# Kernel optimization log

Measured on AMD Instinct MI355X. Metric: run time of the kernel, lower is better.

The kernel has to match this reference:

```python
import jax, jax.numpy as jnp
import numpy as np

B, S, D = 8, 1024, 1024

def setup_inputs() -> dict:
    key = jax.random.key(0)
    ks = jax.random.split(key, 6)
    context = jax.random.normal(ks[0], (B, S, D), dtype=jnp.float32)
    eos_mask = jax.random.randint(ks[1], (B, S), 0, 2, dtype=jnp.int32)
    prior = jax.random.uniform(ks[2], (), dtype=jnp.float32)
    adj_mat = jax.random.randint(ks[3], (B, S, S), 0, 2, dtype=jnp.int32)
    Wk = jax.random.normal(ks[4], (D, D), dtype=jnp.float32) * 0.02
    Wq = jax.random.normal(ks[5], (D, D), dtype=jnp.float32) * 0.02
    bk = jnp.zeros((D,), jnp.float32)
    bq = jnp.zeros((D,), jnp.float32)
    ln_gamma = jnp.ones((D,), jnp.float32)
    ln_beta = jnp.zeros((D,), jnp.float32)
    return {"context": context, "eos_mask": eos_mask, "prior": prior,
            "adj_mat": adj_mat, "Wk": Wk, "bk": bk, "Wq": Wq, "bq": bq,
            "ln_gamma": ln_gamma, "ln_beta": ln_beta}

def reference(context, eos_mask, prior, adj_mat, Wk, bk, Wq, bq, ln_gamma, ln_beta):
    d_model = context.shape[-1]
    seq_len = context.shape[1]
    # LayerNorm (annotated-transformer style: unbiased std, eps added to std)
    mu = jnp.mean(context, axis=-1, keepdims=True)
    std = jnp.std(context, axis=-1, keepdims=True, ddof=1)
    x = ln_gamma * (context - mu) / (std + 1e-6) + ln_beta
    # projections (torch Linear: x @ W.T + b)
    key_p = x @ Wk.T + bk
    query = x @ Wq.T + bq
    scores = jnp.einsum('bqd,bkd->bqk', query, key_p) / (d_model / 2)
    scores = jnp.where(adj_mat == 0, -1e9, scores)
    neibor_attn = jax.nn.softmax(scores, axis=-1)
    neibor_attn = jnp.sqrt(neibor_attn * jnp.swapaxes(neibor_attn, -1, -2) + 1e-9)
    neibor_attn = prior + (1.0 - prior) * neibor_attn
    # constant structural matrices
    a = jnp.eye(seq_len, k=1, dtype=jnp.float32)          # superdiagonal
    b = jnp.eye(seq_len, dtype=jnp.float32)               # diagonal
    tri = jnp.triu(jnp.ones((seq_len, seq_len), jnp.float32))  # upper incl diag
    # t = (log(attn+eps) masked to superdiagonal) @ tri
    t = jnp.matmul(jnp.where(a == 0, 0.0, jnp.log(neibor_attn + 1e-9)), tri)
    g_attn = jnp.exp(jnp.matmul(tri, t))
    g_attn = jnp.where((tri - b) == 0, 0.0, g_attn)  # keep strict upper only
    g_attn = g_attn + jnp.swapaxes(g_attn, -1, -2) + jnp.where(b == 0, 1e-9, neibor_attn)
    return (g_attn, neibor_attn)
```

## Files before the change

kernel.cpp:

```cpp
#include <hip/hip_runtime.h>
#include <hip/hip_bf16.h>

#define S_LEN 1024
#define D_DIM 1024
#define N_BAT 8
#define BSS   (8ull*1024ull*1024ull)

using bf16x8 = __attribute__((ext_vector_type(8))) short;
using f32x4  = __attribute__((ext_vector_type(4))) float;

__device__ __forceinline__ short f2bf(float v) {
    __hip_bfloat16 h = __float2bfloat16(v);
    return *reinterpret_cast<short*>(&h);
}

__device__ __forceinline__ void gload_lds16(const void* g, void* l) {
    __builtin_amdgcn_global_load_lds(
        (const __attribute__((address_space(1))) void*)g,
        (__attribute__((address_space(3))) void*)l, 16, 0, 0);
}

#define RDFRAG(slot, AF, BF)                                                  \
    {                                                                         \
        const char* _Ac = (const char*)As + (slot) * 32768;                   \
        const char* _Bc = (const char*)Bs + (slot) * 16384;                   \
        _Pragma("unroll")                                                     \
        for (int _m = 0; _m < 4; ++_m) {                                      \
            const int _row = wr * 64 + _m * 16 + rsel;                        \
            _Pragma("unroll")                                                 \
            for (int _kk = 0; _kk < 2; ++_kk)                                 \
                AF[_m][_kk] = *(const bf16x8*)&_Ac[_row * 128 +               \
                                                  ((_kk * 64 + kb) ^ sw)];    \
        }                                                                     \
        _Pragma("unroll")                                                     \
        for (int _n = 0; _n < 4; ++_n) {                                      \
            const int _row = wc * 64 + _n * 16 + rsel;                        \
            _Pragma("unroll")                                                 \
            for (int _kk = 0; _kk < 2; ++_kk)                                 \
                BF[_n][_kk] = *(const bf16x8*)&_Bc[_row * 128 +               \
                                                  ((_kk * 64 + kb) ^ sw)];    \
        }                                                                     \
    }

#define MMA_ALL(AF, BF)                                                       \
    __builtin_amdgcn_s_setprio(1);                                            \
    _Pragma("unroll")                                                         \
    for (int _kk = 0; _kk < 2; ++_kk)                                         \
        _Pragma("unroll")                                                     \
        for (int _m = 0; _m < 4; ++_m)                                        \
            _Pragma("unroll")                                                  \
            for (int _n = 0; _n < 4; ++_n)                                    \
                acc[_m][_n] = __builtin_amdgcn_mfma_f32_16x16x32_bf16(        \
                    AF[_m][_kk], BF[_n][_kk], acc[_m][_n], 0, 0, 0);          \
    __builtin_amdgcn_s_setprio(0);

template<int KITERS>
__device__ __forceinline__ void gemm_mainloop256(
    const short* __restrict__ A, const short* __restrict__ Bt,
    int brow, int bcol, int kstart,
    short* As, short* Bs, f32x4 acc[4][4])
{
    const int tid  = threadIdx.x;
    const int lane = tid & 63;
    const int w    = tid >> 6;
    const int wr   = w >> 1;
    const int wc   = w & 1;
    const int rsel = lane & 15;
    const int kb   = (lane >> 4) * 16;
    const int sw   = (rsel & 7) << 4;

    const int srow  = tid >> 3;
    const int scolb = ((tid & 7) * 16) ^ ((srow & 7) << 4);
    const int sdst  = tid * 16;

#pragma unroll
    for (int m = 0; m < 4; ++m)
#pragma unroll
        for (int n = 0; n < 4; ++n) acc[m][n] = 0.0f;

    auto stage = [&](int slot, int k0) {
        char* Ad = (char*)As + slot * 32768;
        char* Bd = (char*)Bs + slot * 16384;
#pragma unroll
        for (int c = 0; c < 4; ++c) {
            const int row = c * 64 + srow;
            gload_lds16((const char*)(A + (size_t)(brow + row) * 1024 + k0) + scolb,
                        Ad + c * 8192 + sdst);
        }
#pragma unroll
        for (int c = 0; c < 2; ++c) {
            const int row = c * 64 + srow;
            gload_lds16((const char*)(Bt + (size_t)(bcol + row) * 1024 + k0) + scolb,
                        Bd + c * 8192 + sdst);
        }
    };

    stage(0, kstart);
    if (KITERS > 1) {
        stage(1, kstart + 64);
        asm volatile("s_waitcnt vmcnt(6)" ::: "memory");
    } else {
        asm volatile("s_waitcnt vmcnt(0)" ::: "memory");
    }
    __builtin_amdgcn_s_barrier();
    asm volatile("" ::: "memory");

    bf16x8 af0[4][2], bf0[4][2], af1[4][2], bf1[4][2];
    RDFRAG(0, af0, bf0);

#pragma unroll
    for (int t = 0; t < KITERS; ++t) {
        if (t + 2 < KITERS) stage((t + 2) % 3, kstart + (t + 2) * 64);
        if (t + 2 < KITERS)      asm volatile("s_waitcnt vmcnt(6)" ::: "memory");
        else if (t + 1 < KITERS) asm volatile("s_waitcnt vmcnt(0)" ::: "memory");
        if (t + 1 < KITERS) {
            asm volatile("s_waitcnt lgkmcnt(0)" ::: "memory");
            __builtin_amdgcn_s_barrier();
            asm volatile("" ::: "memory");
            if ((t & 1) == 0) { RDFRAG((t + 1) % 3, af1, bf1); }
            else              { RDFRAG((t + 1) % 3, af0, bf0); }
        }
        if ((t & 1) == 0) { MMA_ALL(af0, bf0); }
        else              { MMA_ALL(af1, bf1); }
    }
}

__global__ __launch_bounds__(256) void pack_adj(
    const int* __restrict__ adj, unsigned* __restrict__ mb)
{
    const int lane = threadIdx.x & 63;
    const size_t wid = ((size_t)blockIdx.x * 256 + threadIdx.x) >> 6;
    const size_t nw  = ((size_t)gridDim.x * 256) >> 6;
    for (size_t c = wid; c < (BSS >> 6); c += nw) {
        const int a = adj[(c << 6) + lane];
        const unsigned long long m = __ballot(a != 0);
        if ((lane & 31) == 0)
            mb[(c << 1) + (lane >> 5)] = (unsigned)(m >> (lane & 32));
    }
}

__global__ __launch_bounds__(512) void gemm_bf16(
    const short* __restrict__ A, const short* __restrict__ Bt,
    short* __restrict__ C)
{
    __shared__ char smem[147456];
    short* As = (short*)smem;
    short* Bs = (short*)(smem + 98304);
    const int flat = blockIdx.x + 32 * blockIdx.y;
    const int nid  = (flat & 7) * 32 + (flat >> 3);
    const int mx   = nid >> 3;
    const int ny   = nid & 7;
    const int brow = mx * 256, bcol = ny * 128;

    f32x4 acc[4][4];
    gemm_mainloop256<16>(A, Bt, brow, bcol, 0, As, Bs, acc);

    __syncthreads();
    short* ep = (short*)smem;
    const int lane = threadIdx.x & 63;
    const int w    = threadIdx.x >> 6;
    const int wr   = w >> 1, wc = w & 1;
#pragma unroll
    for (int m = 0; m < 4; ++m)
#pragma unroll
        for (int n = 0; n < 4; ++n) {
            const int Cc = wc * 64 + n * 16 + (lane & 15);
#pragma unroll
            for (int r = 0; r < 4; ++r) {
                const int R = wr * 64 + m * 16 + (lane >> 4) * 4 + r;
                ep[R * 136 + Cc] = f2bf(acc[m][n][r]);
            }
        }
    __syncthreads();
#pragma unroll
    for (int it = 0; it < 8; ++it) {
        const int fl  = it * 512 + threadIdx.x;
        const int row = fl >> 4;
        const int c8  = fl & 15;
        const bf16x8 v = *(const bf16x8*)&ep[row * 136 + c8 * 8];
        *(bf16x8*)&C[(size_t)(brow + row) * 1024 + bcol + c8 * 8] = v;
    }
}

__global__ __launch_bounds__(512) void gemm_scores(
    const short* __restrict__ Tm, const short* __restrict__ Xm,
    const float* __restrict__ p, const float* __restrict__ r2,
    const float* __restrict__ c0p, const unsigned* __restrict__ mbase,
    float* __restrict__ Sc)
{
    __shared__ char smem[147456];
    short* As = (short*)smem;
    short* Bs = (short*)(smem + 98304);
    const int flat = blockIdx.x + 4 * blockIdx.y + 32 * blockIdx.z;
    const int nid  = (flat & 7) * 32 + (flat >> 3);
    const int b    = nid >> 5;
    const int rem  = nid & 31;
    const int mx   = rem & 3;
    const int ny   = rem >> 2;
    const short* A  = Tm + (size_t)b * 1024 * 1024;
    const short* Bt = Xm + (size_t)b * 1024 * 1024;
    const float* pb = p  + (size_t)b * 1024;
    const float* rb = r2 + (size_t)b * 1024;
    const unsigned* mbb = mbase + (size_t)b * 32768;
    float* C = Sc + (size_t)b * 1024 * 1024;
    const int brow = mx * 256, bcol = ny * 128;

    f32x4 acc[4][4];
    gemm_mainloop256<16>(A, Bt, brow, bcol, 0, As, Bs, acc);

    __syncthreads();
    float* ep = (float*)smem;
    const int lane = threadIdx.x & 63;
    const int w    = threadIdx.x >> 6;
    const int wr   = w >> 1, wc = w & 1;
#pragma unroll
    for (int m = 0; m < 4; ++m)
#pragma unroll
        for (int n = 0; n < 4; ++n) {
            const int Cc = wc * 64 + n * 16 + (lane & 15);
#pragma unroll
            for (int r = 0; r < 4; ++r) {
                const int R = wr * 64 + m * 16 + (lane >> 4) * 4 + r;
                ep[R * 132 + Cc] = acc[m][n][r];
            }
        }
    __syncthreads();
    const float c0v = c0p[0];
#pragma unroll
    for (int it = 0; it < 16; ++it) {
        const int fl   = it * 512 + threadIdx.x;
        const int row  = fl >> 5;
        const int col4 = fl & 31;
        const int rowg = brow + row;
        const int colg = bcol + col4 * 4;
        float4 v = *(const float4*)&ep[row * 132 + col4 * 4];
        const float4 rv = *(const float4*)&rb[colg];
        const float pa = pb[rowg] + c0v;
        const unsigned mw = mbb[rowg * 32 + (bcol >> 5) + (col4 >> 3)];
        const int j0 = (col4 & 7) * 4;
        v.x = ((mw >> (j0 + 0)) & 1) ? (v.x + pa + rv.x) * 0.001953125f : -1e9f;
        v.y = ((mw >> (j0 + 1)) & 1) ? (v.y + pa + rv.y) * 0.001953125f : -1e9f;
        v.z = ((mw >> (j0 + 2)) & 1) ? (v.z + pa + rv.z) * 0.001953125f : -1e9f;
        v.w = ((mw >> (j0 + 3)) & 1) ? (v.w + pa + rv.w) * 0.001953125f : -1e9f;
        *(float4*)&C[(size_t)rowg * 1024 + colg] = v;
    }
}

__global__ __launch_bounds__(512) void gemm_splitk(
    const short* __restrict__ A, const short* __restrict__ Bt,
    float* __restrict__ P)
{
    __shared__ char smem[147456];
    short* As = (short*)smem;
    short* Bs = (short*)(smem + 98304);
    const int brow = blockIdx.x * 256, bcol = blockIdx.y * 128;
    const int z = blockIdx.z;

    f32x4 acc[4][4];
    gemm_mainloop256<4>(A, Bt, brow, bcol, z * 256, As, Bs, acc);

    float* Pz = P + (size_t)z * 1024 * 1024;
    const int lane = threadIdx.x & 63;
    const int w    = threadIdx.x >> 6;
    const int wr   = w >> 1, wc = w & 1;
#pragma unroll
    for (int m = 0; m < 4; ++m)
#pragma unroll
        for (int n = 0; n < 4; ++n) {
            const int colg = bcol + wc * 64 + n * 16 + (lane & 15);
#pragma unroll
            for (int r = 0; r < 4; ++r) {
                const int rowg = brow + wr * 64 + m * 16 + ((lane >> 4) * 4 + r);
                Pz[(size_t)rowg * 1024 + colg] = acc[m][n][r];
            }
        }
}

__global__ __launch_bounds__(256) void reduce_m2t(
    const float* __restrict__ P, short* __restrict__ M)
{
    const int idx = blockIdx.x * 256 + threadIdx.x;
    const float4* P4 = (const float4*)P;
    float4 s = P4[idx];
    const float4 s1 = P4[idx + 262144];
    const float4 s2 = P4[idx + 524288];
    const float4 s3 = P4[idx + 786432];
    s.x += s1.x + s2.x + s3.x;
    s.y += s1.y + s2.y + s3.y;
    s.z += s1.z + s2.z + s3.z;
    s.w += s1.w + s2.w + s3.w;
    short4 o;
    o.x = f2bf(s.x); o.y = f2bf(s.y); o.z = f2bf(s.z); o.w = f2bf(s.w);
    ((short4*)M)[idx] = o;
}

__global__ __launch_bounds__(256) void bias_gemv1(
    const float* __restrict__ Wq, const float* __restrict__ Wk,
    const float* __restrict__ bk, const float* __restrict__ bq,
    float* __restrict__ pu, float* __restrict__ pv)
{
    __shared__ float su[8][128];
    __shared__ float sv[8][128];
    const int tx = threadIdx.x & 31;
    const int ty = threadIdx.x >> 5;
    const int colBase = blockIdx.x * 128;
    const int rowBase = blockIdx.y * 64;
    const int i = colBase + tx * 4;
    float4 au = {0,0,0,0}, av = {0,0,0,0};
#pragma unroll
    for (int jj = 0; jj < 8; ++jj) {
        const int j = rowBase + ty + jj * 8;
        const float bkv = bk[j], bqv = bq[j];
        const float4 wq = *(const float4*)&Wq[(size_t)j * 1024 + i];
        const float4 wk = *(const float4*)&Wk[(size_t)j * 1024 + i];
        au.x += wq.x * bkv; au.y += wq.y * bkv; au.z += wq.z * bkv; au.w += wq.w * bkv;
        av.x += wk.x * bqv; av.y += wk.y * bqv; av.z += wk.z * bqv; av.w += wk.w * bqv;
    }
    ((float4*)su[ty])[tx] = au;
    ((float4*)sv[ty])[tx] = av;
    __syncthreads();
    if (ty == 0) {
        float4 s1 = ((float4*)su[0])[tx];
        float4 s2 = ((float4*)sv[0])[tx];
#pragma unroll
        for (int k = 1; k < 8; ++k) {
            const float4 t1 = ((float4*)su[k])[tx];
            const float4 t2 = ((float4*)sv[k])[tx];
            s1.x += t1.x; s1.y += t1.y; s1.z += t1.z; s1.w += t1.w;
            s2.x += t2.x; s2.y += t2.y; s2.z += t2.z; s2.w += t2.w;
        }
        ((float4*)&pu[(size_t)blockIdx.y * 1024 + colBase])[tx] = s1;
        ((float4*)&pv[(size_t)blockIdx.y * 1024 + colBase])[tx] = s2;
    }
}

__global__ __launch_bounds__(256) void bias_gemv2(
    const float* __restrict__ pu, const float* __restrict__ pv,
    const float* __restrict__ bk, const float* __restrict__ bq,
    float* __restrict__ u, float* __restrict__ v, float* __restrict__ c0)
{
    __shared__ float sh[4];
    const int i = blockIdx.x * 256 + threadIdx.x;
    float su = 0.0f, sv = 0.0f;
#pragma unroll
    for (int k = 0; k < 16; ++k) {
        su += pu[k * 1024 + i];
        sv += pv[k * 1024 + i];
    }
    u[i] = su;
    v[i] = sv;
    if (blockIdx.x == 0) {
        const int t = threadIdx.x;
        const float4 a = ((const float4*)bq)[t];
        const float4 b = ((const float4*)bk)[t];
        float s = a.x*b.x + a.y*b.y + a.z*b.z + a.w*b.w;
        for (int off = 32; off > 0; off >>= 1) s += __shfl_down(s, off);
        const int lane = t & 63, w = t >> 6;
        if (lane == 0) sh[w] = s;
        __syncthreads();
        if (t == 0) c0[0] = sh[0] + sh[1] + sh[2] + sh[3];
    }
}

__global__ __launch_bounds__(256) void ln_kernel(
    const float* __restrict__ X, const float* __restrict__ gamma,
    const float* __restrict__ beta, const float* __restrict__ u,
    const float* __restrict__ v2, short* __restrict__ Y,
    float* __restrict__ p, float* __restrict__ r2)
{
    __shared__ float sh[16];
    const size_t row = blockIdx.x;
    const int t = threadIdx.x;
    float4 v = ((const float4*)(X + row * 1024))[t];
    float s  = v.x + v.y + v.z + v.w;
    float ss = v.x*v.x + v.y*v.y + v.z*v.z + v.w*v.w;
    for (int off = 32; off > 0; off >>= 1) {
        s  += __shfl_down(s, off);
        ss += __shfl_down(ss, off);
    }
    const int lane = t & 63, w = t >> 6;
    if (lane == 0) { sh[w] = s; sh[4 + w] = ss; }
    __syncthreads();
    if (t == 0) {
        float S  = sh[0] + sh[1] + sh[2] + sh[3];
        float SS = sh[4] + sh[5] + sh[6] + sh[7];
        float mu = S * (1.0f / 1024.0f);
        float var = fmaxf((SS - S * mu) * (1.0f / 1023.0f), 0.0f);
        sh[0] = mu;
        sh[1] = 1.0f / (sqrtf(var) + 1e-6f);
    }
    __syncthreads();
    const float mu = sh[0], inv = sh[1];
    float4 g  = ((const float4*)gamma)[t];
    float4 be = ((const float4*)beta)[t];
    float y0 = g.x * (v.x - mu) * inv + be.x;
    float y1 = g.y * (v.y - mu) * inv + be.y;
    float y2 = g.z * (v.z - mu) * inv + be.z;
    float y3 = g.w * (v.w - mu) * inv + be.w;
    short4 o;
    o.x = f2bf(y0); o.y = f2bf(y1); o.z = f2bf(y2); o.w = f2bf(y3);
    ((short4*)(Y + row * 1024))[t] = o;
    float4 uu = ((const float4*)u)[t];
    float4 vv = ((const float4*)v2)[t];
    float dp = y0*uu.x + y1*uu.y + y2*uu.z + y3*uu.w;
    float dr = y0*vv.x + y1*vv.y + y2*vv.z + y3*vv.w;
    for (int off = 32; off > 0; off >>= 1) {
        dp += __shfl_down(dp, off);
        dr += __shfl_down(dr, off);
    }
    if (lane == 0) { sh[8 + w] = dp; sh[12 + w] = dr; }
    __syncthreads();
    if (t == 0) {
        p[row]  = sh[8] + sh[9] + sh[10] + sh[11];
        r2[row] = sh[12] + sh[13] + sh[14] + sh[15];
    }
}

__global__ __launch_bounds__(256) void cvt_t_kernel(
    const float* __restrict__ Wq, const float* __restrict__ Wk,
    short* __restrict__ wqt, short* __restrict__ wkt)
{
    __shared__ float T[32][33];
    const float* src = blockIdx.z ? Wk : Wq;
    short* dst = blockIdx.z ? wkt : wqt;
    const int bi = blockIdx.x * 32, bj = blockIdx.y * 32;
    const int c = threadIdx.x & 31, r0 = threadIdx.x >> 5;
#pragma unroll
    for (int rr = 0; rr < 4; ++rr) {
        const int r = r0 + rr * 8;
        T[r][c] = src[(size_t)(bi + r) * 1024 + bj + c];
    }
    __syncthreads();
#pragma unroll
    for (int rr = 0; rr < 4; ++rr) {
        const int r = r0 + rr * 8;
        dst[(size_t)(bj + r) * 1024 + bi + c] = f2bf(T[c][r]);
    }
}

__global__ __launch_bounds__(256) void rowstat_kernel(
    const float* __restrict__ Sc, float2* __restrict__ stats)
{
    __shared__ float sh[4];
    const size_t row = blockIdx.x;
    const int t = threadIdx.x;
    const float4 sv = ((const float4*)(Sc + row * 1024))[t];
    float m = fmaxf(fmaxf(sv.x, sv.y), fmaxf(sv.z, sv.w));
    for (int off = 32; off > 0; off >>= 1) m = fmaxf(m, __shfl_down(m, off));
    const int lane = t & 63, w = t >> 6;
    if (lane == 0) sh[w] = m;
    __syncthreads();
    const float M = fmaxf(fmaxf(sh[0], sh[1]), fmaxf(sh[2], sh[3]));
    __syncthreads();
    float s = expf(sv.x - M) + expf(sv.y - M) + expf(sv.z - M) + expf(sv.w - M);
    for (int off = 32; off > 0; off >>= 1) s += __shfl_down(s, off);
    if (lane == 0) sh[w] = s;
    __syncthreads();
    if (t == 0) {
        const float Sm = sh[0] + sh[1] + sh[2] + sh[3];
        stats[row] = make_float2(M, 1.0f / Sm);
    }
}

__global__ __launch_bounds__(1024) void cum2_kernel(
    const float* __restrict__ Sc, const float2* __restrict__ stats,
    const float* __restrict__ prior_p, double* __restrict__ cum)
{
    __shared__ double sh[1024];
    const int b = blockIdx.x;
    const int t = threadIdx.x;
    const float prior = *prior_p;
    const float om = 1.0f - prior;
    const float* sc = Sc + (size_t)b * 1024 * 1024;
    const float2* st = stats + (size_t)b * 1024;
    double v = 0.0;
    if (t >= 1) {
        const int k = t - 1;
        const float2 s1 = st[k], s2 = st[k + 1];
        const float a1 = expf(sc[(size_t)k * 1024 + (k + 1)] - s1.x) * s1.y;
        const float a2 = expf(sc[(size_t)(k + 1) * 1024 + k] - s2.x) * s2.y;
        const float na = prior + om * sqrtf(a1 * a2 + 1e-9f);
        v = (double)logf(na + 1e-9f);
    }
    sh[t] = v;
    __syncthreads();
#pragma unroll
    for (int off = 1; off < 1024; off <<= 1) {
        const double add = (t >= off) ? sh[t - off] : 0.0;
        __syncthreads();
        sh[t] += add;
        __syncthreads();
    }
    cum[b * 1024 + t] = sh[t];
}

__global__ __launch_bounds__(256) void na_g2_kernel(
    float* __restrict__ Sc, const float2* __restrict__ stats,
    const float* __restrict__ prior_p, const double* __restrict__ cum,
    float* __restrict__ NA)
{
    const int flat = blockIdx.x + 1024 * blockIdx.y;
    const int nid  = (flat & 7) * 1024 + (flat >> 3);
    const int b    = nid >> 10;
    const int tidx = nid & 1023;
    const int ti = tidx >> 5, tj = tidx & 31;
    if (tj < ti) return;
    const float prior = *prior_p;
    const float om = 1.0f - prior;
    float* sc = Sc + (size_t)b * 1024 * 1024;
    float* na = NA + (size_t)b * 1024 * 1024;
    const float2* st = stats + (size_t)b * 1024;
    const double* cb = cum + (size_t)b * 1024;
    __shared__ float T1[32][33];
    __shared__ float T2[32][33];
    const int c = threadIdx.x & 31, r0 = threadIdx.x >> 5;
#pragma unroll
    for (int rr = 0; rr < 4; ++rr) {
        const int r = r0 + rr * 8;
        const int R1 = ti * 32 + r, R2 = tj * 32 + r;
        const float2 s1 = st[R1], s2 = st[R2];
        T1[r][c] = expf(sc[(size_t)R1 * 1024 + tj * 32 + c] - s1.x) * s1.y;
        T2[r][c] = expf(sc[(size_t)R2 * 1024 + ti * 32 + c] - s2.x) * s2.y;
    }
    __syncthreads();
#pragma unroll
    for (int rr = 0; rr < 4; ++rr) {
        const int r = r0 + rr * 8;
        const int R1 = ti * 32 + r, C1 = tj * 32 + c;
        const float na1 = prior + om * sqrtf(T1[r][c] * T2[c][r] + 1e-9f);
        na[(size_t)R1 * 1024 + C1] = na1;
        float g1;
        if (R1 == C1) g1 = na1;
        else {
            const int lo = min(R1, C1), hi = max(R1, C1);
            g1 = expf((float)(cb[hi] - cb[lo])) + 1e-9f;
        }
        sc[(size_t)R1 * 1024 + C1] = g1;
        const int R2 = tj * 32 + r, C2 = ti * 32 + c;
        const float na2 = prior + om * sqrtf(T2[r][c] * T1[c][r] + 1e-9f);
        na[(size_t)R2 * 1024 + C2] = na2;
        float g2;
        if (R2 == C2) g2 = na2;
        else {
            const int lo = min(R2, C2), hi = max(R2, C2);
            g2 = expf((float)(cb[hi] - cb[lo])) + 1e-9f;
        }
        sc[(size_t)R2 * 1024 + C2] = g2;
    }
}

extern "C" void kernel_launch(void* const* d_in, const int* in_sizes, int n_in,
                              void* d_out, int out_size, void* d_ws, size_t ws_size,
                              hipStream_t stream)
{
    const float* context = (const float*)d_in[0];
    const float* prior   = (const float*)d_in[2];
    const int*   adj     = (const int*)d_in[3];
    const float* Wk      = (const float*)d_in[4];
    const float* bk      = (const float*)d_in[5];
    const float* Wq      = (const float*)d_in[6];
    const float* bq      = (const float*)d_in[7];
    const float* gamma   = (const float*)d_in[8];
    const float* beta    = (const float*)d_in[9];

    float* out   = (float*)d_out;
    float* gout  = out;
    float* naout = out + BSS;

    char* ws = (char*)d_ws;
    short*  xb    = (short*)(ws);
    short*  wqt   = (short*)(ws + (16ull << 20));
    short*  wkt   = (short*)(ws + (18ull << 20));
    short*  m2t   = (short*)(ws + (20ull << 20));
    short*  tb    = (short*)(ws + (22ull << 20));
    float*  m2par = (float*)tb;
    double* cumd  = (double*)(ws + (38ull << 20));
    float*  uvec  = (float*)(ws + (38ull << 20) + (1ull << 16));
    float*  vvec  = uvec + 1024;
    float*  c0    = vvec + 1024;
    float*  pvec  = c0 + 64;
    float*  rvec  = pvec + 8192;
    float*  pu    = rvec + 8192;
    float*  pv    = pu + 16384;
    float2* statv = (float2*)(pv + 16384);
    unsigned* mb  = (unsigned*)(ws + (39ull << 20));

    pack_adj<<<2048, 256, 0, stream>>>(adj, mb);
    bias_gemv1<<<dim3(8, 16), 256, 0, stream>>>(Wq, Wk, bk, bq, pu, pv);
    bias_gemv2<<<4, 256, 0, stream>>>(pu, pv, bk, bq, uvec, vvec, c0);
    ln_kernel<<<8192, 256, 0, stream>>>(context, gamma, beta, uvec, vvec,
                                        xb, pvec, rvec);
    cvt_t_kernel<<<dim3(32, 32, 2), 256, 0, stream>>>(Wq, Wk, wqt, wkt);
    gemm_splitk<<<dim3(4, 8, 4), 512, 0, stream>>>(wkt, wqt, m2par);
    reduce_m2t<<<1024, 256, 0, stream>>>(m2par, m2t);
    gemm_bf16<<<dim3(32, 8), 512, 0, stream>>>(xb, m2t, tb);
    gemm_scores<<<dim3(4, 8, 8), 512, 0, stream>>>(tb, xb, pvec, rvec, c0,
                                                   mb, gout);
    rowstat_kernel<<<8192, 256, 0, stream>>>(gout, statv);
    cum2_kernel<<<8, 1024, 0, stream>>>(gout, statv, prior, cumd);
    na_g2_kernel<<<dim3(1024, 8), 256, 0, stream>>>(gout, statv, prior, cumd,
                                                    naout);
}
```

Before: 126.2 us.

## Fuse adjacency masking and partial softmax stats into scores GEMM epilogue

Removes the separate pack_adj kernel and reads the int adjacency matrix directly in the scores GEMM epilogue. The epilogue also computes per-row online max/sum-exp partials across each 128-column tile and writes them out. A tiny rowstat2 kernel merges the 8 partials per row, replacing the full rowstat pass that reread the 32MB score matrix. This trades a 32MB adj read (same as before, but now inside the GEMM epilogue) and extra shuffles/exps in the epilogue for dropping one full score read and a kernel launch.

```diff
diff --git a/kernel.cpp b/kernel.cpp
--- a/kernel.cpp
+++ b/kernel.cpp
@@ -125,20 +125,6 @@
     }
 }
 
-__global__ __launch_bounds__(256) void pack_adj(
-    const int* __restrict__ adj, unsigned* __restrict__ mb)
-{
-    const int lane = threadIdx.x & 63;
-    const size_t wid = ((size_t)blockIdx.x * 256 + threadIdx.x) >> 6;
-    const size_t nw  = ((size_t)gridDim.x * 256) >> 6;
-    for (size_t c = wid; c < (BSS >> 6); c += nw) {
-        const int a = adj[(c << 6) + lane];
-        const unsigned long long m = __ballot(a != 0);
-        if ((lane & 31) == 0)
-            mb[(c << 1) + (lane >> 5)] = (unsigned)(m >> (lane & 32));
-    }
-}
-
 __global__ __launch_bounds__(512) void gemm_bf16(
     const short* __restrict__ A, const short* __restrict__ Bt,
     short* __restrict__ C)
@@ -185,8 +171,8 @@
 __global__ __launch_bounds__(512) void gemm_scores(
     const short* __restrict__ Tm, const short* __restrict__ Xm,
     const float* __restrict__ p, const float* __restrict__ r2,
-    const float* __restrict__ c0p, const unsigned* __restrict__ mbase,
-    float* __restrict__ Sc)
+    const float* __restrict__ c0p, const int* __restrict__ adj,
+    float* __restrict__ Sc, float2* __restrict__ pstats)
 {
     __shared__ char smem[147456];
     short* As = (short*)smem;
@@ -201,7 +187,7 @@
     const short* Bt = Xm + (size_t)b * 1024 * 1024;
     const float* pb = p  + (size_t)b * 1024;
     const float* rb = r2 + (size_t)b * 1024;
-    const unsigned* mbb = mbase + (size_t)b * 32768;
+    const int*   ab = adj + (size_t)b * 1024 * 1024;
     float* C = Sc + (size_t)b * 1024 * 1024;
     const int brow = mx * 256, bcol = ny * 128;
 
@@ -226,6 +212,7 @@
         }
     __syncthreads();
     const float c0v = c0p[0];
+    const size_t growbase = (size_t)b * 1024 + brow;
 #pragma unroll
     for (int it = 0; it < 16; ++it) {
         const int fl   = it * 512 + threadIdx.x;
@@ -236,13 +223,25 @@
         float4 v = *(const float4*)&ep[row * 132 + col4 * 4];
         const float4 rv = *(const float4*)&rb[colg];
         const float pa = pb[rowg] + c0v;
-        const unsigned mw = mbb[rowg * 32 + (bcol >> 5) + (col4 >> 3)];
-        const int j0 = (col4 & 7) * 4;
-        v.x = ((mw >> (j0 + 0)) & 1) ? (v.x + pa + rv.x) * 0.001953125f : -1e9f;
-        v.y = ((mw >> (j0 + 1)) & 1) ? (v.y + pa + rv.y) * 0.001953125f : -1e9f;
-        v.z = ((mw >> (j0 + 2)) & 1) ? (v.z + pa + rv.z) * 0.001953125f : -1e9f;
-        v.w = ((mw >> (j0 + 3)) & 1) ? (v.w + pa + rv.w) * 0.001953125f : -1e9f;
+        const int4 av = *(const int4*)&ab[(size_t)rowg * 1024 + colg];
+        v.x = av.x ? (v.x + pa + rv.x) * 0.001953125f : -1e9f;
+        v.y = av.y ? (v.y + pa + rv.y) * 0.001953125f : -1e9f;
+        v.z = av.z ? (v.z + pa + rv.z) * 0.001953125f : -1e9f;
+        v.w = av.w ? (v.w + pa + rv.w) * 0.001953125f : -1e9f;
         *(float4*)&C[(size_t)rowg * 1024 + colg] = v;
+        float cm = fmaxf(fmaxf(v.x, v.y), fmaxf(v.z, v.w));
+        float cs = expf(v.x - cm) + expf(v.y - cm) +
+                   expf(v.z - cm) + expf(v.w - cm);
+#pragma unroll
+        for (int off = 1; off < 32; off <<= 1) {
+            const float om = __shfl_xor(cm, off);
+            const float os = __shfl_xor(cs, off);
+            const float nm = fmaxf(cm, om);
+            cs = cs * expf(cm - nm) + os * expf(om - nm);
+            cm = nm;
+        }
+        if ((threadIdx.x & 31) == 0)
+            pstats[(growbase + row) * 8 + ny] = make_float2(cm, cs);
     }
 }
 
@@ -438,28 +437,19 @@
     }
 }
 
-__global__ __launch_bounds__(256) void rowstat_kernel(
-    const float* __restrict__ Sc, float2* __restrict__ stats)
-{
-    __shared__ float sh[4];
-    const size_t row = blockIdx.x;
-    const int t = threadIdx.x;
-    const float4 sv = ((const float4*)(Sc + row * 1024))[t];
-    float m = fmaxf(fmaxf(sv.x, sv.y), fmaxf(sv.z, sv.w));
-    for (int off = 32; off > 0; off >>= 1) m = fmaxf(m, __shfl_down(m, off));
-    const int lane = t & 63, w = t >> 6;
-    if (lane == 0) sh[w] = m;
-    __syncthreads();
-    const float M = fmaxf(fmaxf(sh[0], sh[1]), fmaxf(sh[2], sh[3]));
-    __syncthreads();
-    float s = expf(sv.x - M) + expf(sv.y - M) + expf(sv.z - M) + expf(sv.w - M);
-    for (int off = 32; off > 0; off >>= 1) s += __shfl_down(s, off);
-    if (lane == 0) sh[w] = s;
-    __syncthreads();
-    if (t == 0) {
-        const float Sm = sh[0] + sh[1] + sh[2] + sh[3];
-        stats[row] = make_float2(M, 1.0f / Sm);
-    }
+__global__ __launch_bounds__(256) void rowstat2(
+    const float2* __restrict__ ps, float2* __restrict__ stats)
+{
+    const int row = blockIdx.x * 256 + threadIdx.x;
+    float M = -3.4e38f, S = 0.0f;
+#pragma unroll
+    for (int j = 0; j < 8; ++j) {
+        const float2 q = ps[(size_t)row * 8 + j];
+        const float nm = fmaxf(M, q.x);
+        S = S * expf(M - nm) + q.y * expf(q.x - nm);
+        M = nm;
+    }
+    stats[row] = make_float2(M, 1.0f / S);
 }
 
 __global__ __launch_bounds__(1024) void cum2_kernel(
@@ -583,9 +573,8 @@
     float*  pu    = rvec + 8192;
     float*  pv    = pu + 16384;
     float2* statv = (float2*)(pv + 16384);
-    unsigned* mb  = (unsigned*)(ws + (39ull << 20));
-
-    pack_adj<<<2048, 256, 0, stream>>>(adj, mb);
+    float2* psts  = (float2*)(ws + (39ull << 20));
+
     bias_gemv1<<<dim3(8, 16), 256, 0, stream>>>(Wq, Wk, bk, bq, pu, pv);
     bias_gemv2<<<4, 256, 0, stream>>>(pu, pv, bk, bq, uvec, vvec, c0);
     ln_kernel<<<8192, 256, 0, stream>>>(context, gamma, beta, uvec, vvec,
@@ -595,8 +584,8 @@
     reduce_m2t<<<1024, 256, 0, stream>>>(m2par, m2t);
     gemm_bf16<<<dim3(32, 8), 512, 0, stream>>>(xb, m2t, tb);
     gemm_scores<<<dim3(4, 8, 8), 512, 0, stream>>>(tb, xb, pvec, rvec, c0,
-                                                   mb, gout);
-    rowstat_kernel<<<8192, 256, 0, stream>>>(gout, statv);
+                                                   adj, gout, psts);
+    rowstat2<<<32, 256, 0, stream>>>(psts, statv);
     cum2_kernel<<<8, 1024, 0, stream>>>(gout, statv, prior, cumd);
     na_g2_kernel<<<dim3(1024, 8), 256, 0, stream>>>(gout, statv, prior, cumd,
                                                     naout);
```

Measured after the change: 138.9 us. 1.1x slower.
